# Optimization experiments

Measured on AMD Instinct MI355X. Metric: run time of the kernel, lower is better.

Reference implementation:

```python
import jax, jax.numpy as jnp
import numpy as np

B, S, IN = 16, 512, 32
D, H, L = 768, 12, 6
DH = D // H
DFF = 4 * D
EPS = 1e-5
NEG = -1e9


def _ln(x, g, b):
    m = jnp.mean(x, axis=-1, keepdims=True)
    v = jnp.mean(jnp.square(x - m), axis=-1, keepdims=True)
    return (x - m) * jax.lax.rsqrt(v + EPS) * g + b


def setup_inputs() -> dict:
    key = jax.random.key(0)
    ks = jax.random.split(key, 24)
    nrm = lambda k, shape, s=0.02: jax.random.normal(k, shape, jnp.float32) * s
    inp = {
        'x': jax.random.normal(ks[0], (B, S, IN), jnp.float32),
        'event_lengths': jax.random.randint(ks[1], (B,), 1, S + 1),
        'in_w': nrm(ks[2], (IN, D)),
        'in_b': jnp.zeros((D,), jnp.float32),
        'pos_emb': nrm(ks[3], (S, D)),
        'qw': nrm(ks[4], (L, D, D)), 'qb': jnp.zeros((L, D), jnp.float32),
        'kw': nrm(ks[5], (L, D, D)), 'kb': jnp.zeros((L, D), jnp.float32),
        'vw': nrm(ks[6], (L, D, D)), 'vb': jnp.zeros((L, D), jnp.float32),
        'w1': nrm(ks[7], (L, D, DFF)), 'b1': jnp.zeros((L, DFF), jnp.float32),
        'w2': nrm(ks[8], (L, DFF, D)), 'b2': jnp.zeros((L, D), jnp.float32),
        'ln1_g': jnp.ones((L, D), jnp.float32), 'ln1_b': jnp.zeros((L, D), jnp.float32),
        'ln2_g': jnp.ones((L, D), jnp.float32), 'ln2_b': jnp.zeros((L, D), jnp.float32),
        'out_w': nrm(ks[9], (D, 1)), 'out_b': jnp.zeros((1,), jnp.float32),
    }
    return inp


def reference(x, event_lengths, in_w, in_b, pos_emb, qw, qb, kw, kb, vw, vb,
              w1, b1, w2, b2, ln1_g, ln1_b, ln2_g, ln2_b, out_w, out_b):
    b, s, _ = x.shape
    h = x @ in_w + in_b + pos_emb[None, :s]  # [B,S,D]
    valid = jnp.arange(s)[None, :] < event_lengths[:, None]  # [B,S]
    amask = valid[:, None, :, None] & valid[:, None, None, :]  # [B,1,S,S]
    scale = np.float32(1.0 / np.sqrt(DH))
    for l in range(qw.shape[0]):
        q = (h @ qw[l] + qb[l]).reshape(b, s, H, DH)
        k = (h @ kw[l] + kb[l]).reshape(b, s, H, DH)
        v = (h @ vw[l] + vb[l]).reshape(b, s, H, DH)
        scores = jnp.einsum('bqhd,bkhd->bhqk', q, k) * scale
        scores = jnp.where(amask, scores, NEG)
        p = jax.nn.softmax(scores, axis=-1)
        o = jnp.einsum('bhqk,bkhd->bqhd', p, v).reshape(b, s, -1)
        # NOTE: source overwrites summarize(...) output with the raw concat, so no out-proj
        h = _ln(h + o, ln1_g[l], ln1_b[l])
        ff = jnp.maximum(h @ w1[l] + b1[l], 0.0) @ w2[l] + b2[l]
        h = _ln(h + ff, ln2_g[l], ln2_b[l])
    pooled = jnp.where(valid[..., None], h, 0.0).sum(axis=1) / event_lengths[:, None].astype(h.dtype)
    return pooled @ out_w + out_b  # [B,1]
```

## Files before the change

### kernel.cpp

```cpp
#include <hip/hip_runtime.h>

typedef unsigned short u16;
typedef unsigned int u32;
typedef u16 u16x8 __attribute__((ext_vector_type(8)));
typedef u16 u16x4 __attribute__((ext_vector_type(4)));
typedef __bf16 bf16x8 __attribute__((ext_vector_type(8)));
typedef float f32x4 __attribute__((ext_vector_type(4)));

#define DEV __device__ __forceinline__

DEV u16 f2bf(float f) {
  u32 u = __builtin_bit_cast(u32, f);
  u32 r = u + 0x7fffu + ((u >> 16) & 1u);
  return (u16)(r >> 16);
}

DEV float bf2f(u16 v) { return __builtin_bit_cast(float, (u32)v << 16); }

DEV int imin(int a, int b) { return a < b ? a : b; }

DEV void gload_lds16(const void* g, void* l) {
  __builtin_amdgcn_global_load_lds(
      (const __attribute__((address_space(1))) void*)g,
      (__attribute__((address_space(3))) void*)l, 16, 0, 0);
}

template <int RELU, int VMODE, int PIPE, int BM, int BN>
__global__ __launch_bounds__(256, (PIPE && BM == 128) ? 2 : 3) void gemm97_kernel(
    const u16* __restrict__ A, const u16* __restrict__ Bt, const float* __restrict__ bias,
    u16* __restrict__ Cb, u16* __restrict__ vT, const int* __restrict__ lens, int M, int N, int K,
    int ldc) {
  constexpr int MF = BM / 32;
  constexpr int NF = BN / 32;
  constexpr int ASZ = BM * 64;
  constexpr int BSZ = BN * 64;
  __shared__ __align__(16) u16 SB[PIPE ? 2 * ASZ + 2 * BSZ : ASZ + BSZ];
  const int t = threadIdx.x, wave = t >> 6, lane = t & 63;
  const int fr = lane & 15, fq = lane >> 4;
  const int NT = K >> 6;
  const int nbx = N / BN;

  int bid = blockIdx.x;
  {
    const int cpx = (int)gridDim.x >> 3;
    bid = (bid & 7) * cpx + (bid >> 3);
  }
  const int bx = bid % nbx, by = bid / nbx;
  const int m0 = by * BM, n0 = bx * BN;
  if ((m0 & 511) >= lens[m0 >> 9]) return;

  const int srow = t >> 3;
  const int c8 = ((t & 7) ^ (srow & 7)) * 8;
  const u16* ag = A + (size_t)(m0 + srow) * K + c8;
  const u16* bg = Bt + (size_t)(n0 + srow) * K + c8;

  auto STAGE = [&](int buf, int kt) {
    char* a = (char*)(SB + (PIPE ? buf * ASZ : 0)) + wave * 1024;
    char* b = (char*)(SB + (PIPE ? 2 * ASZ + buf * BSZ : ASZ)) + wave * 1024;
    const u16* agp = ag + (size_t)kt * 64;
    const u16* bgp = bg + (size_t)kt * 64;
#pragma unroll
    for (int i = 0; i < MF; ++i) gload_lds16(agp + (size_t)i * 32 * K, a + i * 4096);
#pragma unroll
    for (int i = 0; i < NF; ++i) gload_lds16(bgp + (size_t)i * 32 * K, b + i * 4096);
  };

  const int wr = (wave >> 1) * (BM / 2), wc = (wave & 1) * (BN / 2);
  f32x4 acc[MF][NF] = {};

  if (PIPE) {
    STAGE(0, 0);
    asm volatile("s_waitcnt vmcnt(0)" ::: "memory");
    __syncthreads();
  }

  for (int kt = 0; kt < NT; ++kt) {
    const int cur = PIPE ? (kt & 1) : 0;
    if (PIPE) {
      if (kt + 1 < NT) STAGE(cur ^ 1, kt + 1);
    } else {
      STAGE(0, kt);
      asm volatile("s_waitcnt vmcnt(0)" ::: "memory");
      __syncthreads();
    }
    const u16* Ab = SB + (PIPE ? cur * ASZ : 0);
    const u16* Bb = SB + (PIPE ? 2 * ASZ + cur * BSZ : ASZ);
#pragma unroll
    for (int ks = 0; ks < 2; ++ks) {
      bf16x8 af[MF], bv[NF];
#pragma unroll
      for (int m = 0; m < MF; ++m)
        af[m] = *(const bf16x8*)(Ab + (wr + m * 16 + fr) * 64 + (((ks * 4 + fq) ^ (fr & 7)) * 8));
#pragma unroll
      for (int n = 0; n < NF; ++n)
        bv[n] = *(const bf16x8*)(Bb + (wc + n * 16 + fr) * 64 + (((ks * 4 + fq) ^ (fr & 7)) * 8));
#pragma unroll
      for (int m = 0; m < MF; ++m)
#pragma unroll
        for (int n = 0; n < NF; ++n)
          acc[m][n] = __builtin_amdgcn_mfma_f32_16x16x32_bf16(af[m], bv[n], acc[m][n], 0, 0, 0);
    }
    if (PIPE) asm volatile("s_waitcnt vmcnt(0)" ::: "memory");
    __syncthreads();
  }

  if (VMODE && n0 >= 1536) {
#pragma unroll
    for (int n = 0; n < NF; ++n) {
      const int col = n0 + wc + n * 16 + fr;
      const float bvv = bias[col];
      const int dd = col - 1536;
      const int hh = dd >> 6, d6 = dd & 63;
#pragma unroll
      for (int m = 0; m < MF; ++m) {
        const int row0 = m0 + wr + m * 16 + fq * 4;
        const int bb = row0 >> 9, ss = row0 & 511;
        u16x4 pk;
#pragma unroll
        for (int r = 0; r < 4; ++r) pk[r] = f2bf(acc[m][n][r] + bvv);
        *(u16x4*)(vT + ((size_t)(bb * 12 + hh) * 64 + d6) * 512 + ss) = pk;
      }
    }
  } else {
#pragma unroll
    for (int n = 0; n < NF; ++n) {
      const int col = wc + n * 16 + fr;
      const float bvv = bias[n0 + col];
#pragma unroll
      for (int m = 0; m < MF; ++m) {
#pragma unroll
        for (int r = 0; r < 4; ++r) {
          const int row = wr + m * 16 + fq * 4 + r;
          float v = acc[m][n][r] + bvv;
          if (RELU) v = fmaxf(v, 0.f);
          SB[row * BN + (col ^ ((row & 7) << 4))] = f2bf(v);
        }
      }
    }
    __syncthreads();
    constexpr int TPR = BN / 8;
    constexpr int RPP = 256 / TPR;
#pragma unroll
    for (int i = 0; i < BM / RPP; ++i) {
      const int row = (t / TPR) + i * RPP;
      const int col8 = (t % TPR) * 8;
      u16x8 vv = *(const u16x8*)(SB + row * BN + (col8 ^ ((row & 7) << 4)));
      *(u16x8*)(Cb + (size_t)(m0 + row) * ldc + n0 + col8) = vv;
    }
  }
}

__global__ __launch_bounds__(256) void attn_kernel(const u16* __restrict__ qk,
                                                   const u16* __restrict__ vT,
                                                   const int* __restrict__ lens,
                                                   u16* __restrict__ o) {
  __shared__ __align__(16) u16 Kl[128 * 64];
  __shared__ __align__(16) u16 Vt[64 * 128];
  __shared__ __align__(16) u16 Pl[4][16 * 128];

  const int bid = blockIdx.x;
  const int qq = bid & 3;
  const int pair = bid >> 2;
  const int h = pair % 12;
  const int b = pair / 12;
  const int len = lens[b];
  if (qq * 128 >= len) return;
  const int t = threadIdx.x, wave = t >> 6, lane = t & 63;
  const int fr = lane & 15, fq = lane >> 4;

  const size_t base = (size_t)b * 512 * 1536;
  const size_t vbase = (size_t)(b * 12 + h) * 64 * 512;
  const int q0w = qq * 128 + wave * 32;

  bf16x8 qf[2][2];
#pragma unroll
  for (int qi = 0; qi < 2; ++qi)
#pragma unroll
    for (int ks = 0; ks < 2; ++ks)
      qf[qi][ks] = *(const bf16x8*)(qk + base + (size_t)(q0w + qi * 16 + fr) * 1536 + h * 64 +
                                    ks * 32 + fq * 8);

  f32x4 oacc[2][4] = {};
  float mrow[2][4], lrow[2][4];
#pragma unroll
  for (int qi = 0; qi < 2; ++qi)
#pragma unroll
    for (int r = 0; r < 4; ++r) {
      mrow[qi][r] = -1e30f;
      lrow[qi][r] = 0.f;
    }

  const int nt = (len + 127) >> 7;
  for (int kt = 0; kt < nt; ++kt) {
    const int kv0 = kt * 128;
#pragma unroll
    for (int i = 0; i < 4; ++i) {
      const int c = i * 256 + t;
      const int krow = c >> 3, kch = c & 7;
      u16x8 kvl = *(const u16x8*)(qk + base + (size_t)(kv0 + krow) * 1536 + 768 + h * 64 + kch * 8);
      *(u16x8*)(Kl + krow * 64 + ((kch ^ (krow & 7)) * 8)) = kvl;
      const int d = c >> 4, vch = c & 15;
      u16x8 vv = *(const u16x8*)(vT + vbase + (size_t)d * 512 + kv0 + vch * 8);
      *(u16x8*)(Vt + d * 128 + ((vch ^ (d & 7)) * 8)) = vv;
    }
    __syncthreads();

#pragma unroll
    for (int qi = 0; qi < 2; ++qi) {
      if (q0w + qi * 16 >= len) break;
      f32x4 sa[8] = {};
#pragma unroll
      for (int ks = 0; ks < 2; ++ks) {
#pragma unroll
        for (int n = 0; n < 8; ++n) {
          const int colr = n * 16 + fr;
          bf16x8 kf = *(const bf16x8*)(Kl + colr * 64 + (((ks * 4 + fq) ^ (colr & 7)) * 8));
          sa[n] = __builtin_amdgcn_mfma_f32_16x16x32_bf16(qf[qi][ks], kf, sa[n], 0, 0, 0);
        }
      }

      float tm[4] = {-1e30f, -1e30f, -1e30f, -1e30f};
#pragma unroll
      for (int n = 0; n < 8; ++n) {
        const int col = kv0 + n * 16 + fr;
        const bool ok = col < len;
#pragma unroll
        for (int r = 0; r < 4; ++r) {
          const float s = ok ? sa[n][r] * 0.125f : -1e30f;
          sa[n][r] = s;
          tm[r] = fmaxf(tm[r], s);
        }
      }
#pragma unroll
      for (int d = 1; d < 16; d <<= 1)
#pragma unroll
        for (int r = 0; r < 4; ++r) tm[r] = fmaxf(tm[r], __shfl_xor(tm[r], d));

      float al[4], rs[4];
#pragma unroll
      for (int r = 0; r < 4; ++r) {
        const float mn = fmaxf(mrow[qi][r], tm[r]);
        al[r] = __expf(mrow[qi][r] - mn);
        mrow[qi][r] = mn;
        rs[r] = 0.f;
      }
#pragma unroll
      for (int n = 0; n < 8; ++n)
#pragma unroll
        for (int r = 0; r < 4; ++r) {
          const float p = __expf(sa[n][r] - mrow[qi][r]);
          sa[n][r] = p;
          rs[r] += p;
        }
#pragma unroll
      for (int d = 1; d < 16; d <<= 1)
#pragma unroll
        for (int r = 0; r < 4; ++r) rs[r] += __shfl_xor(rs[r], d);
#pragma unroll
      for (int r = 0; r < 4; ++r) lrow[qi][r] = lrow[qi][r] * al[r] + rs[r];
#pragma unroll
      for (int n = 0; n < 4; ++n)
#pragma unroll
        for (int r = 0; r < 4; ++r) oacc[qi][n][r] *= al[r];

      u16* P = &Pl[wave][0];
#pragma unroll
      for (int n = 0; n < 8; ++n) {
        const int col = n * 16 + fr;
#pragma unroll
        for (int r = 0; r < 4; ++r) {
          const int row = fq * 4 + r;
          P[row * 128 + (((col >> 3) ^ (row & 7)) * 8) + (col & 7)] = f2bf(sa[n][r]);
        }
      }
#pragma unroll
      for (int kslot = 0; kslot < 4; ++kslot) {
        const int ch = kslot * 4 + fq;
        bf16x8 pa = *(const bf16x8*)(P + fr * 128 + ((ch ^ (fr & 7)) * 8));
#pragma unroll
        for (int n = 0; n < 4; ++n) {
          const int colv = n * 16 + fr;
          bf16x8 vf = *(const bf16x8*)(Vt + colv * 128 + ((ch ^ (colv & 7)) * 8));
          oacc[qi][n] = __builtin_amdgcn_mfma_f32_16x16x32_bf16(pa, vf, oacc[qi][n], 0, 0, 0);
        }
      }
    }
    __syncthreads();
  }

  const size_t obase = (size_t)b * 512 * 768 + (size_t)q0w * 768 + h * 64;
#pragma unroll
  for (int qi = 0; qi < 2; ++qi) {
    if (q0w + qi * 16 >= len) break;
#pragma unroll
    for (int n = 0; n < 4; ++n)
#pragma unroll
      for (int r = 0; r < 4; ++r)
        o[obase + (size_t)(qi * 16 + fq * 4 + r) * 768 + n * 16 + fr] =
            f2bf(oacc[qi][n][r] / lrow[qi][r]);
  }
}

__global__ __launch_bounds__(256) void transpose_all_kernel(
    const float* __restrict__ qw, const float* __restrict__ kw, const float* __restrict__ vw,
    const float* __restrict__ w1, const float* __restrict__ w2, u16* __restrict__ qkvt6,
    u16* __restrict__ w1t6, u16* __restrict__ w2t6) {
  __shared__ float tile[64][65];
  const int l = blockIdx.y;
  int x = blockIdx.x;
  const float* in;
  u16* op;
  int K, N, nbx;
  if (x < 432) {
    const int which = x / 144;
    x -= which * 144;
    in = (which == 0 ? qw : which == 1 ? kw : vw) + (size_t)l * 768 * 768;
    op = qkvt6 + (size_t)l * 2304 * 768 + (size_t)which * 768 * 768;
    K = 768;
    N = 768;
    nbx = 12;
  } else if (x < 1008) {
    x -= 432;
    in = w1 + (size_t)l * 768 * 3072;
    op = w1t6 + (size_t)l * 3072 * 768;
    K = 768;
    N = 3072;
    nbx = 48;
  } else {
    x -= 1008;
    in = w2 + (size_t)l * 3072 * 768;
    op = w2t6 + (size_t)l * 768 * 3072;
    K = 3072;
    N = 768;
    nbx = 12;
  }
  const int tx = threadIdx.x & 63, ty = threadIdx.x >> 6;
  const int n0 = (x % nbx) * 64, k0 = (x / nbx) * 64;
#pragma unroll
  for (int i = 0; i < 16; ++i)
    tile[ty + i * 4][tx] = in[(size_t)(k0 + ty + i * 4) * N + n0 + tx];
  __syncthreads();
#pragma unroll
  for (int i = 0; i < 16; ++i)
    op[(size_t)(n0 + ty + i * 4) * K + k0 + tx] = f2bf(tile[tx][ty + i * 4]);
}

__global__ __launch_bounds__(256) void inproj_kernel(const float* __restrict__ x,
                                                     const float* __restrict__ in_w,
                                                     const float* __restrict__ in_b,
                                                     const float* __restrict__ pos,
                                                     u16* __restrict__ hbf) {
  __shared__ float xs[8][32];
  const int t = threadIdx.x;
  const int row0 = blockIdx.x * 8;
  xs[t >> 5][t & 31] = x[(size_t)row0 * 32 + t];
  __syncthreads();
#pragma unroll
  for (int j = 0; j < 3; ++j) {
    const int d = t + j * 256;
    float acc[8] = {};
#pragma unroll
    for (int i = 0; i < 32; ++i) {
      const float wv = in_w[i * 768 + d];
#pragma unroll
      for (int r = 0; r < 8; ++r) acc[r] += xs[r][i] * wv;
    }
    const float bb = in_b[d];
#pragma unroll
    for (int r = 0; r < 8; ++r) {
      const int row = row0 + r;
      const int s = row & 511;
      hbf[(size_t)row * 768 + d] = f2bf(acc[r] + bb + pos[(size_t)s * 768 + d]);
    }
  }
}

__global__ __launch_bounds__(256) void ln_kernel(u16* __restrict__ hbf,
                                                 const u16* __restrict__ delta,
                                                 const int* __restrict__ lens,
                                                 const float* __restrict__ g,
                                                 const float* __restrict__ bb) {
  const int row = blockIdx.x * 4 + (threadIdx.x >> 6);
  if ((row & 511) >= lens[row >> 9]) return;
  const int lane = threadIdx.x & 63;
  const size_t rb = (size_t)row * 768 + lane * 4;
  f32x4 xv[3];
  float s = 0.f, s2 = 0.f;
#pragma unroll
  for (int j = 0; j < 3; ++j) {
    u16x4 a = *(const u16x4*)(hbf + rb + j * 256);
    u16x4 dv = *(const u16x4*)(delta + rb + j * 256);
    f32x4 v;
#pragma unroll
    for (int c = 0; c < 4; ++c) v[c] = bf2f(a[c]) + bf2f(dv[c]);
    xv[j] = v;
    s += v[0] + v[1] + v[2] + v[3];
    s2 += v[0] * v[0] + v[1] * v[1] + v[2] * v[2] + v[3] * v[3];
  }
#pragma unroll
  for (int d = 1; d < 64; d <<= 1) {
    s += __shfl_xor(s, d);
    s2 += __shfl_xor(s2, d);
  }
  const float mean = s * (1.f / 768.f);
  const float var = fmaxf(s2 * (1.f / 768.f) - mean * mean, 0.f);
  const float rstd = rsqrtf(var + 1e-5f);
#pragma unroll
  for (int j = 0; j < 3; ++j) {
    f32x4 gv = *(const f32x4*)(g + lane * 4 + j * 256);
    f32x4 bv = *(const f32x4*)(bb + lane * 4 + j * 256);
    u16x4 yb;
#pragma unroll
    for (int c = 0; c < 4; ++c) yb[c] = f2bf((xv[j][c] - mean) * rstd * gv[c] + bv[c]);
    *(u16x4*)(hbf + rb + j * 256) = yb;
  }
}

__global__ __launch_bounds__(256) void pool1_kernel(const u16* __restrict__ h,
                                                    const int* __restrict__ lens,
                                                    const float* __restrict__ ow,
                                                    float* __restrict__ wsp) {
  const int b = blockIdx.x >> 3, chunk = blockIdx.x & 7;
  const int len = lens[b];
  const int t = threadIdx.x;
  const int s0 = chunk * 64;
  const int s1 = imin(s0 + 64, len);
  float acc0 = 0.f, acc1 = 0.f, acc2 = 0.f;
  const u16* hp = h + (size_t)b * 512 * 768;
  for (int s = s0; s < s1; ++s) {
    const size_t rb = (size_t)s * 768;
    acc0 += bf2f(hp[rb + t]);
    acc1 += bf2f(hp[rb + t + 256]);
    acc2 += bf2f(hp[rb + t + 512]);
  }
  float part = acc0 * ow[t] + acc1 * ow[t + 256] + acc2 * ow[t + 512];
#pragma unroll
  for (int d = 1; d < 64; d <<= 1) part += __shfl_xor(part, d);
  __shared__ float ps[4];
  if ((t & 63) == 0) ps[t >> 6] = part;
  __syncthreads();
  if (t == 0) wsp[blockIdx.x] = ps[0] + ps[1] + ps[2] + ps[3];
}

__global__ void pool2_kernel(const float* __restrict__ wsp, const int* __restrict__ lens,
                             const float* __restrict__ ob, float* __restrict__ out) {
  const int b = threadIdx.x;
  if (b < 16) {
    float s = 0.f;
#pragma unroll
    for (int c = 0; c < 8; ++c) s += wsp[b * 8 + c];
    out[b] = s / (float)lens[b] + ob[0];
  }
}

__global__ void biaspack_kernel(const float* __restrict__ qb, const float* __restrict__ kb,
                                const float* __restrict__ vb, float* __restrict__ qkvb) {
  const int i = blockIdx.x * 256 + threadIdx.x;
  if (i >= 6 * 2304) return;
  const int l = i / 2304, j = i % 2304;
  float v;
  if (j < 768)
    v = qb[l * 768 + j];
  else if (j < 1536)
    v = kb[l * 768 + j - 768];
  else
    v = vb[l * 768 + j - 1536];
  qkvb[i] = v;
}

extern "C" void kernel_launch(void* const* d_in, const int* in_sizes, int n_in, void* d_out,
                              int out_size, void* d_ws, size_t ws_size, hipStream_t stream) {
  const float* x = (const float*)d_in[0];
  const int* lens = (const int*)d_in[1];
  const float* in_w = (const float*)d_in[2];
  const float* in_b = (const float*)d_in[3];
  const float* pos = (const float*)d_in[4];
  const float* qw = (const float*)d_in[5];
  const float* qb = (const float*)d_in[6];
  const float* kw = (const float*)d_in[7];
  const float* kb = (const float*)d_in[8];
  const float* vw = (const float*)d_in[9];
  const float* vb = (const float*)d_in[10];
  const float* w1 = (const float*)d_in[11];
  const float* b1 = (const float*)d_in[12];
  const float* w2 = (const float*)d_in[13];
  const float* b2 = (const float*)d_in[14];
  const float* ln1g = (const float*)d_in[15];
  const float* ln1b = (const float*)d_in[16];
  const float* ln2g = (const float*)d_in[17];
  const float* ln2b = (const float*)d_in[18];
  const float* ow = (const float*)d_in[19];
  const float* ob = (const float*)d_in[20];
  float* out = (float*)d_out;

  char* w = (char*)d_ws;
  size_t off = 0;
  auto alloc = [&](size_t bytes) -> void* {
    void* p = w + off;
    off += (bytes + 255) & ~(size_t)255;
    return p;
  };
  u16* qkvt6 = (u16*)alloc((size_t)6 * 2304 * 768 * 2);
  u16* w1t6 = (u16*)alloc((size_t)6 * 3072 * 768 * 2);
  u16* w2t6 = (u16*)alloc((size_t)6 * 768 * 3072 * 2);
  float* qkvb = (float*)alloc((size_t)6 * 2304 * 4);
  u16* hbf = (u16*)alloc((size_t)8192 * 768 * 2);
  u16* obuf = (u16*)alloc((size_t)8192 * 768 * 2);
  u16* ubuf = (u16*)alloc((size_t)8192 * 3072 * 2);
  float* wsp = (float*)alloc((size_t)128 * 4);
  u16* qkbuf = ubuf;
  u16* vT = ubuf + (size_t)8192 * 1536;
  u16* ffbuf = ubuf;

  biaspack_kernel<<<(6 * 2304 + 255) / 256, 256, 0, stream>>>(qb, kb, vb, qkvb);
  transpose_all_kernel<<<dim3(1584, 6), 256, 0, stream>>>(qw, kw, vw, w1, w2, qkvt6, w1t6, w2t6);
  inproj_kernel<<<1024, 256, 0, stream>>>(x, in_w, in_b, pos, hbf);

  for (int l = 0; l < 6; ++l) {
    gemm97_kernel<0, 1, 0, 64, 128><<<2304, 256, 0, stream>>>(
        hbf, qkvt6 + (size_t)l * 2304 * 768, qkvb + l * 2304, qkbuf, vT, lens, 8192, 2304, 768,
        1536);
    attn_kernel<<<768, 256, 0, stream>>>(qkbuf, vT, lens, obuf);
    ln_kernel<<<2048, 256, 0, stream>>>(hbf, obuf, lens, ln1g + l * 768, ln1b + l * 768);
    gemm97_kernel<1, 0, 0, 64, 256><<<1536, 256, 0, stream>>>(
        hbf, w1t6 + (size_t)l * 3072 * 768, b1 + l * 3072, ffbuf, nullptr, lens, 8192, 3072, 768,
        3072);
    gemm97_kernel<0, 0, 1, 64, 128><<<768, 256, 0, stream>>>(
        ffbuf, w2t6 + (size_t)l * 768 * 3072, b2 + l * 768, obuf, nullptr, lens, 8192, 768, 3072,
        768);
    ln_kernel<<<2048, 256, 0, stream>>>(hbf, obuf, lens, ln2g + l * 768, ln2b + l * 768);
  }
  pool1_kernel<<<128, 256, 0, stream>>>(hbf, lens, ow, wsp);
  pool2_kernel<<<1, 64, 0, stream>>>(wsp, lens, ob, out);
  (void)in_sizes;
  (void)n_in;
  (void)out_size;
  (void)ws_size;
}
```

Measured before the change: 1.142 ms.

## Split-K the FFN down-projection into two partials summed in LayerNorm

```diff
diff --git a/kernel.cpp b/kernel.cpp
--- a/kernel.cpp
+++ b/kernel.cpp
@@ -28,8 +28,8 @@
 template <int RELU, int VMODE, int PIPE, int BM, int BN>
 __global__ __launch_bounds__(256, (PIPE && BM == 128) ? 2 : 3) void gemm97_kernel(
     const u16* __restrict__ A, const u16* __restrict__ Bt, const float* __restrict__ bias,
-    u16* __restrict__ Cb, u16* __restrict__ vT, const int* __restrict__ lens, int M, int N, int K,
-    int ldc) {
+    u16* __restrict__ Cb, u16* __restrict__ vT, const int* __restrict__ lens, int M, int N,
+    int ksub, int ld, int nsplit, int ldc) {
   constexpr int MF = BM / 32;
   constexpr int NF = BN / 32;
   constexpr int ASZ = BM * 64;
@@ -37,22 +37,25 @@
   __shared__ __align__(16) u16 SB[PIPE ? 2 * ASZ + 2 * BSZ : ASZ + BSZ];
   const int t = threadIdx.x, wave = t >> 6, lane = t & 63;
   const int fr = lane & 15, fq = lane >> 4;
-  const int NT = K >> 6;
+  const int NT = ksub >> 6;
   const int nbx = N / BN;
+  const int tiles = nbx * (M / BM);
 
   int bid = blockIdx.x;
   {
     const int cpx = (int)gridDim.x >> 3;
     bid = (bid & 7) * cpx + (bid >> 3);
   }
+  const int sp = bid / tiles;
+  bid -= sp * tiles;
   const int bx = bid % nbx, by = bid / nbx;
   const int m0 = by * BM, n0 = bx * BN;
   if ((m0 & 511) >= lens[m0 >> 9]) return;
 
   const int srow = t >> 3;
   const int c8 = ((t & 7) ^ (srow & 7)) * 8;
-  const u16* ag = A + (size_t)(m0 + srow) * K + c8;
-  const u16* bg = Bt + (size_t)(n0 + srow) * K + c8;
+  const u16* ag = A + (size_t)sp * ksub + (size_t)(m0 + srow) * ld + c8;
+  const u16* bg = Bt + (size_t)sp * ksub + (size_t)(n0 + srow) * ld + c8;
 
   auto STAGE = [&](int buf, int kt) {
     char* a = (char*)(SB + (PIPE ? buf * ASZ : 0)) + wave * 1024;
@@ -60,9 +63,9 @@
     const u16* agp = ag + (size_t)kt * 64;
     const u16* bgp = bg + (size_t)kt * 64;
 #pragma unroll
-    for (int i = 0; i < MF; ++i) gload_lds16(agp + (size_t)i * 32 * K, a + i * 4096);
-#pragma unroll
-    for (int i = 0; i < NF; ++i) gload_lds16(bgp + (size_t)i * 32 * K, b + i * 4096);
+    for (int i = 0; i < MF; ++i) gload_lds16(agp + (size_t)i * 32 * ld, a + i * 4096);
+#pragma unroll
+    for (int i = 0; i < NF; ++i) gload_lds16(bgp + (size_t)i * 32 * ld, b + i * 4096);
   };
 
   const int wr = (wave >> 1) * (BM / 2), wc = (wave & 1) * (BN / 2);
@@ -125,7 +128,7 @@
 #pragma unroll
     for (int n = 0; n < NF; ++n) {
       const int col = wc + n * 16 + fr;
-      const float bvv = bias[n0 + col];
+      const float bvv = (nsplit == 1 || sp == 0) ? bias[n0 + col] : 0.f;
 #pragma unroll
       for (int m = 0; m < MF; ++m) {
 #pragma unroll
@@ -140,12 +143,13 @@
     __syncthreads();
     constexpr int TPR = BN / 8;
     constexpr int RPP = 256 / TPR;
+    u16* Cp = Cb + (size_t)sp * M * ldc;
 #pragma unroll
     for (int i = 0; i < BM / RPP; ++i) {
       const int row = (t / TPR) + i * RPP;
       const int col8 = (t % TPR) * 8;
       u16x8 vv = *(const u16x8*)(SB + row * BN + (col8 ^ ((row & 7) << 4)));
-      *(u16x8*)(Cb + (size_t)(m0 + row) * ldc + n0 + col8) = vv;
+      *(u16x8*)(Cp + (size_t)(m0 + row) * ldc + n0 + col8) = vv;
     }
   }
 }
@@ -375,8 +379,10 @@
   }
 }
 
+template <int ND>
 __global__ __launch_bounds__(256) void ln_kernel(u16* __restrict__ hbf,
-                                                 const u16* __restrict__ delta,
+                                                 const u16* __restrict__ d0,
+                                                 const u16* __restrict__ d1,
                                                  const int* __restrict__ lens,
                                                  const float* __restrict__ g,
                                                  const float* __restrict__ bb) {
@@ -389,10 +395,15 @@
 #pragma unroll
   for (int j = 0; j < 3; ++j) {
     u16x4 a = *(const u16x4*)(hbf + rb + j * 256);
-    u16x4 dv = *(const u16x4*)(delta + rb + j * 256);
+    u16x4 dv = *(const u16x4*)(d0 + rb + j * 256);
     f32x4 v;
 #pragma unroll
     for (int c = 0; c < 4; ++c) v[c] = bf2f(a[c]) + bf2f(dv[c]);
+    if (ND == 2) {
+      u16x4 ev = *(const u16x4*)(d1 + rb + j * 256);
+#pragma unroll
+      for (int c = 0; c < 4; ++c) v[c] += bf2f(ev[c]);
+    }
     xv[j] = v;
     s += v[0] + v[1] + v[2] + v[3];
     s2 += v[0] * v[0] + v[1] * v[1] + v[2] * v[2] + v[3] * v[3];
@@ -505,7 +516,7 @@
   u16* w2t6 = (u16*)alloc((size_t)6 * 768 * 3072 * 2);
   float* qkvb = (float*)alloc((size_t)6 * 2304 * 4);
   u16* hbf = (u16*)alloc((size_t)8192 * 768 * 2);
-  u16* obuf = (u16*)alloc((size_t)8192 * 768 * 2);
+  u16* obuf = (u16*)alloc((size_t)2 * 8192 * 768 * 2);
   u16* ubuf = (u16*)alloc((size_t)8192 * 3072 * 2);
   float* wsp = (float*)alloc((size_t)128 * 4);
   u16* qkbuf = ubuf;
@@ -519,16 +530,18 @@
   for (int l = 0; l < 6; ++l) {
     gemm97_kernel<0, 1, 0, 64, 128><<<2304, 256, 0, stream>>>(
         hbf, qkvt6 + (size_t)l * 2304 * 768, qkvb + l * 2304, qkbuf, vT, lens, 8192, 2304, 768,
-        1536);
+        768, 1, 1536);
     attn_kernel<<<768, 256, 0, stream>>>(qkbuf, vT, lens, obuf);
-    ln_kernel<<<2048, 256, 0, stream>>>(hbf, obuf, lens, ln1g + l * 768, ln1b + l * 768);
+    ln_kernel<1><<<2048, 256, 0, stream>>>(hbf, obuf, nullptr, lens, ln1g + l * 768,
+                                           ln1b + l * 768);
     gemm97_kernel<1, 0, 0, 64, 256><<<1536, 256, 0, stream>>>(
         hbf, w1t6 + (size_t)l * 3072 * 768, b1 + l * 3072, ffbuf, nullptr, lens, 8192, 3072, 768,
-        3072);
-    gemm97_kernel<0, 0, 1, 64, 128><<<768, 256, 0, stream>>>(
-        ffbuf, w2t6 + (size_t)l * 768 * 3072, b2 + l * 768, obuf, nullptr, lens, 8192, 768, 3072,
-        768);
-    ln_kernel<<<2048, 256, 0, stream>>>(hbf, obuf, lens, ln2g + l * 768, ln2b + l * 768);
+        768, 1, 3072);
+    gemm97_kernel<0, 0, 0, 64, 128><<<1536, 256, 0, stream>>>(
+        ffbuf, w2t6 + (size_t)l * 768 * 3072, b2 + l * 768, obuf, nullptr, lens, 8192, 768, 1536,
+        3072, 2, 768);
+    ln_kernel<2><<<2048, 256, 0, stream>>>(hbf, obuf, obuf + (size_t)8192 * 768, lens,
+                                           ln2g + l * 768, ln2b + l * 768);
   }
   pool1_kernel<<<128, 256, 0, stream>>>(hbf, lens, ow, wsp);
   pool2_kernel<<<1, 64, 0, stream>>>(wsp, lens, ob, out);
```

Result: no change. 1.145 ms (+0.2%).
